# Kernel tuning notes

Measured on AMD Instinct MI355X. Metric: run time of the kernel, lower is better.

## Reference

```python
import jax, jax.numpy as jnp
import numpy as np

NUM_TAGS = 512
START_TAG = 510
STOP_TAG = 511
BATCH = 128
SEQ_LEN = 512
NEG_INF = -10000.0


def setup_inputs() -> dict:
    key = jax.random.key(0)
    k1, k2, k3 = jax.random.split(key, 3)
    inputs = jax.random.normal(k1, (BATCH, SEQ_LEN, NUM_TAGS), dtype=jnp.float32)
    tags = jax.random.randint(k2, (BATCH, SEQ_LEN), 0, NUM_TAGS)
    transitions = jax.random.normal(k3, (NUM_TAGS, NUM_TAGS), dtype=jnp.float32)
    # match the torch __init__ sentinel masking of the transition matrix
    transitions = transitions.at[START_TAG, :].set(NEG_INF)
    transitions = transitions.at[:, STOP_TAG].set(NEG_INF)
    return {"inputs": inputs, "tags": tags, "transitions": transitions}


def reference(inputs, tags, transitions):
    # inputs: [B, S, T] emission scores; transitions[j, i] = score of i -> j
    B, S, T = inputs.shape
    alpha0 = jnp.full((B, T), NEG_INF, dtype=inputs.dtype)
    alpha0 = alpha0.at[:, START_TAG].set(0.0)

    def step(alpha, emit):
        # alpha: [B, T] (prev tags), emit: [B, T] (next tags)
        # scores[b, next, prev] = alpha[b, prev] + transitions[next, prev]
        scores = alpha[:, None, :] + transitions[None, :, :]  # [B, T, T]
        new_alpha = emit + jax.nn.logsumexp(scores, axis=-1)   # [B, T]
        return new_alpha, None

    emits = jnp.moveaxis(inputs, 1, 0)  # [S, B, T]
    alpha, _ = jax.lax.scan(step, alpha0, emits)

    terminal = alpha + transitions[STOP_TAG][None, :]  # [B, T]
    losses = jax.nn.logsumexp(terminal, axis=-1)       # [B]
    return jnp.sum(losses)
```

## Files before the change

kernel.cpp:

```cpp
#include <hip/hip_runtime.h>
#include <stdint.h>

#define NTAGS 512
#define STAG 510
#define PTAG 511
#define SEQ 512
#define L2E 1.4426950408889634f
#define LN2 0.6931471805599453f

typedef int   v8i __attribute__((ext_vector_type(8)));
typedef float v4f __attribute__((ext_vector_type(4)));

__device__ __forceinline__ float fexp2(float x) {
#if __has_builtin(__builtin_amdgcn_exp2f)
    return __builtin_amdgcn_exp2f(x);
#else
    float r; asm("v_exp_f32 %0, %1\n\ts_nop 1" : "=v"(r) : "v"(x)); return r;
#endif
}

#define DPPMAX(X, CTRL) fmaxf((X), __int_as_float(__builtin_amdgcn_update_dpp( \
    0, __float_as_int(X), (CTRL), 0xF, 0xF, false)))

#define STEP_SYNC() asm volatile("s_waitcnt lgkmcnt(0)\n\ts_barrier" ::: "memory")

#define WS_SC   196608
#define WS_PART 204800

__global__ void crf_setup_k(const float* __restrict__ trans, uint8_t* __restrict__ ws)
{
    int t = blockIdx.x * blockDim.x + threadIdx.x;
    int n = t >> 4, KB = t & 15;
    const float* row = trans + n * NTAGS;
    int wq = KB >> 1, h = KB & 1;
    float v[32]; float mx = -3.0e38f;
    #pragma unroll
    for (int k = 0; k < 32; ++k) {
        int p = wq*64 + (k & 3)*16 + h*8 + (k >> 2);
        v[k] = row[p]; mx = fmaxf(mx, v[k]);
    }
    int e = (int)floorf(mx * L2E - 2.90689059f);
    int byt = e + 127; byt = byt < 0 ? 0 : (byt > 254 ? 254 : byt);
    float eeff = (float)(byt - 127);
    uint32_t out[6] = {0u,0u,0u,0u,0u,0u};
    #pragma unroll
    for (int k = 0; k < 32; ++k) {
        float q = exp2f(v[k] * L2E - eeff);
        int code;
        if      (q < 2.0f) code = (int)(q * 8.0f + 0.5f);
        else if (q < 4.0f) code = 16 + (int)((q - 2.0f) * 4.0f + 0.5f);
        else               code = 24 + (int)((q - 4.0f) * 2.0f + 0.5f);
        code = code > 31 ? 31 : code;
        int bp = 6*k, d = bp >> 5, off = bp & 31;
        out[d] |= (uint32_t)code << off;
        if (off > 26) out[d+1] |= (uint32_t)code >> (32 - off);
    }
    uint32_t* E6 = (uint32_t*)ws;
    int base = (n*16 + KB) * 6;
    #pragma unroll
    for (int d = 0; d < 6; ++d) E6[base + d] = out[d];
    ws[WS_SC + n*16 + (KB & 3)*4 + (KB >> 2)] = (uint8_t)byt;
}

__global__ __launch_bounds__(512, 2) void crf_main_k(
    const float* __restrict__ inp, const float* __restrict__ trans,
    const uint8_t* __restrict__ ws, float* __restrict__ part)
{
    __shared__ uint8_t aqb[2*8192];
    __shared__ uint8_t scb[2*256];
    __shared__ int     mxp[2*16];
    __shared__ float   mxb[16*8];
    __shared__ float   ssum[16*8];
    __shared__ float   Gb[16];

    const int tid = threadIdx.x;
    const int w = tid >> 6, l = tid & 63, c = l & 15, g = l >> 4;
    const int wg = blockIdx.x;
    const int b0 = g * 4;

    v8i Bf[16];
    int esc[4];
    #pragma unroll
    for (int i = 0; i < 4; ++i) {
        const int n = (w*4 + i)*16 + c;
        esc[i] = *(const int*)(ws + WS_SC + n*16 + g*4);
        #pragma unroll
        for (int kk = 0; kk < 4; ++kk) {
            const uint2* p2 = (const uint2*)((const uint32_t*)ws + (n*16 + kk*4 + g)*6);
            uint2 d0 = p2[0], d1 = p2[1], d2 = p2[2];
            v8i bv;
            bv[0]=(int)d0.x; bv[1]=(int)d0.y; bv[2]=(int)d1.x;
            bv[3]=(int)d1.y; bv[4]=(int)d2.x; bv[5]=(int)d2.y;
            bv[6]=0; bv[7]=0;
            Bf[i*4 + kk] = bv;
        }
    }
    #pragma unroll
    for (int i = 0; i < 16; ++i) asm volatile("" : "+v"(Bf[i]));
    #pragma unroll
    for (int i = 0; i < 4; ++i)  asm volatile("" : "+v"(esc[i]));

    const float* ep[4];
    #pragma unroll
    for (int j = 0; j < 4; ++j)
        ep[j] = inp + (size_t)(wg*16 + b0 + j) * (SEQ*NTAGS) + w*64 + c;

    int aqoff[4], scoffw[4];
    #pragma unroll
    for (int j = 0; j < 4; ++j) {
        int bb = b0 + j;
        aqoff[j] = bb*128 + (((w*4 + (c>>2)) ^ (bb & 7)) << 2) + (c & 3);
        int B_ = w*2 + (c>>3);
        scoffw[j] = bb*16 + ((B_ & 3)<<2) + (B_>>2);
    }

#define QUANT_STORE(J, V0, V1, V2, V3, RJ, AQ, SC) do { \
    float bm_ = fmaxf(fmaxf(V0, V1), fmaxf(V2, V3)); \
    bm_ = DPPMAX(bm_, 0xB1); bm_ = DPPMAX(bm_, 0x4E); bm_ = DPPMAX(bm_, 0x141); \
    int be_ = (int)((__float_as_uint(bm_) >> 23) & 255u) - 127; \
    be_ = be_ < -60 ? -60 : be_; \
    float qs_ = __int_as_float((uint32_t)(133 - be_) << 23); \
    int t_ = __builtin_amdgcn_cvt_pk_fp8_f32((V0)*qs_, (V1)*qs_, 0, false); \
    t_ = __builtin_amdgcn_cvt_pk_fp8_f32((V2)*qs_, (V3)*qs_, t_, true); \
    ((uint32_t*)(AQ))[aqoff[J]] = (uint32_t)t_; \
    if ((c & 7) == 0) { \
        int sb_ = 121 + be_ - (RJ); sb_ = sb_ < 0 ? 0 : (sb_ > 254 ? 254 : sb_); \
        (SC)[scoffw[J]] = (uint8_t)sb_; \
    } \
    bmout_[J] = bm_; \
} while (0)

    float vv[4][4];
    {
        float tr[4];
        #pragma unroll
        for (int i = 0; i < 4; ++i) tr[i] = trans[(w*64 + i*16 + c)*NTAGS + STAG];
        #pragma unroll
        for (int j = 0; j < 4; ++j) {
            #pragma unroll
            for (int i = 0; i < 4; ++i)
                vv[j][i] = ep[j][i*16] + tr[i];
        }
    }
    float Mj[4];
    #pragma unroll
    for (int j = 0; j < 4; ++j) {
        float m = fmaxf(fmaxf(vv[j][0], vv[j][1]), fmaxf(vv[j][2], vv[j][3]));
        #pragma unroll
        for (int msk = 1; msk <= 8; msk <<= 1) m = fmaxf(m, __shfl_xor(m, msk, 64));
        if (c == 0) mxb[(b0 + j)*8 + w] = m;
    }
    __syncthreads();
    float G[4];
    #pragma unroll
    for (int j = 0; j < 4; ++j) {
        float m = -3.0e38f;
        #pragma unroll
        for (int k = 0; k < 8; ++k) m = fmaxf(m, mxb[(b0 + j)*8 + k]);
        Mj[j] = m;
        G[j] = m * L2E;
    }
    {
        float bmout_[4];
        uint8_t* AQ = aqb + 8192; uint8_t* SC = scb + 256;
        #pragma unroll
        for (int j = 0; j < 4; ++j) {
            float q0 = fexp2((vv[j][0] - Mj[j]) * L2E);
            float q1 = fexp2((vv[j][1] - Mj[j]) * L2E);
            float q2 = fexp2((vv[j][2] - Mj[j]) * L2E);
            float q3 = fexp2((vv[j][3] - Mj[j]) * L2E);
            QUANT_STORE(j, q0, q1, q2, q3, 0, AQ, SC);
        }
        (void)bmout_;
    }
    if (w == 0 && c == 0) { int4 z; z.x=0; z.y=0; z.z=0; z.w=0; *(int4*)&mxp[16 + g*4] = z; }

    float emn[4][4];
    #pragma unroll
    for (int j = 0; j < 4; ++j) ep[j] += NTAGS;
    #pragma unroll
    for (int j = 0; j < 4; ++j) {
        #pragma unroll
        for (int i = 0; i < 4; ++i) emn[j][i] = ep[j][i*16];
    }
    __syncthreads();

    int aoffA[8];
    #pragma unroll
    for (int kk = 0; kk < 4; ++kk) {
        aoffA[2*kk]   = c*32 + ((kk*8 + g*2)     ^ (c & 7));
        aoffA[2*kk+1] = c*32 + ((kk*8 + g*2 + 1) ^ (c & 7));
    }
    const int scoff = c*16 + g*4;

#define MFMA_K(KK) do { \
    v8i A_; \
    *(int4*)&A_       = aq4[aoffA[2*(KK)]]; \
    *(((int4*)&A_)+1) = aq4[aoffA[2*(KK)+1]]; \
    D[0] = __builtin_amdgcn_mfma_scale_f32_16x16x128_f8f6f4(A_, Bf[0*4+(KK)], D[0], 0, 2, (KK), scA, (KK), esc[0]); \
    D[1] = __builtin_amdgcn_mfma_scale_f32_16x16x128_f8f6f4(A_, Bf[1*4+(KK)], D[1], 0, 2, (KK), scA, (KK), esc[1]); \
    D[2] = __builtin_amdgcn_mfma_scale_f32_16x16x128_f8f6f4(A_, Bf[2*4+(KK)], D[2], 0, 2, (KK), scA, (KK), esc[2]); \
    D[3] = __builtin_amdgcn_mfma_scale_f32_16x16x128_f8f6f4(A_, Bf[3*4+(KK)], D[3], 0, 2, (KK), scA, (KK), esc[3]); \
} while (0)

    for (int s = 1; s < SEQ; ++s) {
        const int cur = s & 1, nxt = cur ^ 1;

        float emx[4][4];
        #pragma unroll
        for (int j = 0; j < 4; ++j) {
            #pragma unroll
            for (int i = 0; i < 4; ++i) emx[j][i] = fexp2(emn[j][i] * L2E);
        }
        if (s < SEQ - 1) {
            #pragma unroll
            for (int j = 0; j < 4; ++j) ep[j] += NTAGS;
            #pragma unroll
            for (int j = 0; j < 4; ++j) {
                #pragma unroll
                for (int i = 0; i < 4; ++i) emn[j][i] = ep[j][i*16];
            }
        }

        int4 Pv = *(const int4*)&mxp[cur*16 + g*4];
        uint32_t scA = *(const uint32_t*)(scb + cur*256 + scoff);
        const int4* aq4 = (const int4*)(aqb + cur*8192);

        v4f D[4];
        #pragma unroll
        for (int i = 0; i < 4; ++i) { D[i][0]=0.f; D[i][1]=0.f; D[i][2]=0.f; D[i][3]=0.f; }
        __builtin_amdgcn_s_setprio(1);
        MFMA_K(0); MFMA_K(1); MFMA_K(2); MFMA_K(3);
        __builtin_amdgcn_s_setprio(0);

        if (s < SEQ - 1) {
            int Rj[4];
            #pragma unroll
            for (int j = 0; j < 4; ++j) {
                Rj[j] = ((const int*)&Pv)[j] + 8;
                G[j] += (float)Rj[j];
            }
            float bmout_[4];
            uint8_t* AQ = aqb + nxt*8192; uint8_t* SC = scb + nxt*256;
            #pragma unroll
            for (int j = 0; j < 4; ++j) {
                float v0 = D[0][j] * emx[j][0];
                float v1 = D[1][j] * emx[j][1];
                float v2 = D[2][j] * emx[j][2];
                float v3 = D[3][j] * emx[j][3];
                QUANT_STORE(j, v0, v1, v2, v3, Rj[j], AQ, SC);
            }
            if (w == 0) {
                int4 post;
                #pragma unroll
                for (int j = 0; j < 4; ++j) {
                    float bb = DPPMAX(bmout_[j], 0x140);
                    int be0 = (int)((__float_as_uint(bb) >> 23) & 255u) - 127;
                    ((int*)&post)[j] = be0 - Rj[j];
                }
                if (c == 0) *(int4*)&mxp[nxt*16 + g*4] = post;
            }
            STEP_SYNC();
        } else {
            float ts[4];
            #pragma unroll
            for (int i = 0; i < 4; ++i) ts[i] = trans[PTAG*NTAGS + w*64 + i*16 + c];
            float x[4][4];
            #pragma unroll
            for (int j = 0; j < 4; ++j) {
                #pragma unroll
                for (int i = 0; i < 4; ++i)
                    x[j][i] = __log2f(D[i][j]) + (emn[j][i] + ts[i]) * L2E;
            }
            #pragma unroll
            for (int j = 0; j < 4; ++j) {
                float m = fmaxf(fmaxf(x[j][0], x[j][1]), fmaxf(x[j][2], x[j][3]));
                #pragma unroll
                for (int msk = 1; msk <= 8; msk <<= 1) m = fmaxf(m, __shfl_xor(m, msk, 64));
                if (c == 0) mxb[(b0 + j)*8 + w] = m;
            }
            if (w == 0 && c == 0) {
                #pragma unroll
                for (int j = 0; j < 4; ++j) Gb[b0 + j] = G[j];
            }
            __syncthreads();
            #pragma unroll
            for (int j = 0; j < 4; ++j) {
                float XM = -3.0e38f;
                #pragma unroll
                for (int k = 0; k < 8; ++k) XM = fmaxf(XM, mxb[(b0 + j)*8 + k]);
                float sj = fexp2(x[j][0] - XM) + fexp2(x[j][1] - XM)
                         + fexp2(x[j][2] - XM) + fexp2(x[j][3] - XM);
                #pragma unroll
                for (int msk = 1; msk <= 8; msk <<= 1) sj += __shfl_xor(sj, msk, 64);
                if (c == 0) ssum[(b0 + j)*8 + w] = sj;
            }
            __syncthreads();
            if (tid < 16) {
                float S = 0.f, XM = -3.0e38f;
                #pragma unroll
                for (int k = 0; k < 8; ++k) { S += ssum[tid*8 + k]; XM = fmaxf(XM, mxb[tid*8 + k]); }
                part[wg*16 + tid] = LN2 * (Gb[tid] + XM + __log2f(S));
            }
        }
    }
#undef MFMA_K
#undef QUANT_STORE
}

__global__ void crf_final_k(const float* __restrict__ part, float* __restrict__ out)
{
    int t = threadIdx.x;
    float vsum = part[t] + part[t + 64];
    #pragma unroll
    for (int off = 32; off; off >>= 1) vsum += __shfl_down(vsum, off, 64);
    if (t == 0) out[0] = vsum;
}

extern "C" void kernel_launch(void* const* d_in, const int* in_sizes, int n_in,
                              void* d_out, int out_size, void* d_ws, size_t ws_size,
                              hipStream_t stream)
{
    (void)in_sizes; (void)n_in; (void)out_size; (void)ws_size;
    const float* inp   = (const float*)d_in[0];
    const float* trans = (const float*)d_in[2];
    uint8_t* ws = (uint8_t*)d_ws;
    float* part = (float*)(ws + WS_PART);

    crf_setup_k<<<64, 128, 0, stream>>>(trans, ws);
    crf_main_k<<<8, 512, 0, stream>>>(inp, trans, ws, part);
    crf_final_k<<<1, 64, 0, stream>>>(part, (float*)d_out);
}
```

Baseline: 790.9 us.

## Replace per-block A scales with constant scale and per-row exponent folded into emissions

Removes the per-8-column block-exponent scaling of the alpha vector (the scb shared array, its per-step writes and reads, and the per-lane block max reductions). Each batch row now gets one power-of-two shift, derived from the previous step's row max plus a margin, which is folded into the emission exponent via an fma. The fp8 A operand uses a fixed scale constant and values are clamped at 448. This shortens the per-step critical path (fewer DPP reductions and LDS traffic), but only wave 0 still computes the row max, and the coarser per-row scaling risks precision loss or underflow for small entries.

```diff
diff --git a/kernel.cpp b/kernel.cpp
--- a/kernel.cpp
+++ b/kernel.cpp
@@ -7,6 +7,7 @@
 #define SEQ 512
 #define L2E 1.4426950408889634f
 #define LN2 0.6931471805599453f
+#define MARGIN 13
 
 typedef int   v8i __attribute__((ext_vector_type(8)));
 typedef float v4f __attribute__((ext_vector_type(4)));
@@ -67,7 +68,6 @@
     const uint8_t* __restrict__ ws, float* __restrict__ part)
 {
     __shared__ uint8_t aqb[2*8192];
-    __shared__ uint8_t scb[2*256];
     __shared__ int     mxp[2*16];
     __shared__ float   mxb[16*8];
     __shared__ float   ssum[16*8];
@@ -77,6 +77,7 @@
     const int w = tid >> 6, l = tid & 63, c = l & 15, g = l >> 4;
     const int wg = blockIdx.x;
     const int b0 = g * 4;
+    const int SCA = 0x78787878;
 
     v8i Bf[16];
     int esc[4];
@@ -105,30 +106,12 @@
     for (int j = 0; j < 4; ++j)
         ep[j] = inp + (size_t)(wg*16 + b0 + j) * (SEQ*NTAGS) + w*64 + c;
 
-    int aqoff[4], scoffw[4];
+    int aqoff[4];
     #pragma unroll
     for (int j = 0; j < 4; ++j) {
         int bb = b0 + j;
         aqoff[j] = bb*128 + (((w*4 + (c>>2)) ^ (bb & 7)) << 2) + (c & 3);
-        int B_ = w*2 + (c>>3);
-        scoffw[j] = bb*16 + ((B_ & 3)<<2) + (B_>>2);
-    }
-
-#define QUANT_STORE(J, V0, V1, V2, V3, RJ, AQ, SC) do { \
-    float bm_ = fmaxf(fmaxf(V0, V1), fmaxf(V2, V3)); \
-    bm_ = DPPMAX(bm_, 0xB1); bm_ = DPPMAX(bm_, 0x4E); bm_ = DPPMAX(bm_, 0x141); \
-    int be_ = (int)((__float_as_uint(bm_) >> 23) & 255u) - 127; \
-    be_ = be_ < -60 ? -60 : be_; \
-    float qs_ = __int_as_float((uint32_t)(133 - be_) << 23); \
-    int t_ = __builtin_amdgcn_cvt_pk_fp8_f32((V0)*qs_, (V1)*qs_, 0, false); \
-    t_ = __builtin_amdgcn_cvt_pk_fp8_f32((V2)*qs_, (V3)*qs_, t_, true); \
-    ((uint32_t*)(AQ))[aqoff[J]] = (uint32_t)t_; \
-    if ((c & 7) == 0) { \
-        int sb_ = 121 + be_ - (RJ); sb_ = sb_ < 0 ? 0 : (sb_ > 254 ? 254 : sb_); \
-        (SC)[scoffw[J]] = (uint8_t)sb_; \
-    } \
-    bmout_[J] = bm_; \
-} while (0)
+    }
 
     float vv[4][4];
     {
@@ -161,17 +144,17 @@
         G[j] = m * L2E;
     }
     {
-        float bmout_[4];
-        uint8_t* AQ = aqb + 8192; uint8_t* SC = scb + 256;
+        uint32_t* AQ = (uint32_t*)(aqb + 8192);
         #pragma unroll
         for (int j = 0; j < 4; ++j) {
-            float q0 = fexp2((vv[j][0] - Mj[j]) * L2E);
-            float q1 = fexp2((vv[j][1] - Mj[j]) * L2E);
-            float q2 = fexp2((vv[j][2] - Mj[j]) * L2E);
-            float q3 = fexp2((vv[j][3] - Mj[j]) * L2E);
-            QUANT_STORE(j, q0, q1, q2, q3, 0, AQ, SC);
-        }
-        (void)bmout_;
+            float q0 = fexp2((vv[j][0] - Mj[j]) * L2E + 7.0f);
+            float q1 = fexp2((vv[j][1] - Mj[j]) * L2E + 7.0f);
+            float q2 = fexp2((vv[j][2] - Mj[j]) * L2E + 7.0f);
+            float q3 = fexp2((vv[j][3] - Mj[j]) * L2E + 7.0f);
+            int t_ = __builtin_amdgcn_cvt_pk_fp8_f32(q0, q1, 0, false);
+            t_ = __builtin_amdgcn_cvt_pk_fp8_f32(q2, q3, t_, true);
+            AQ[aqoff[j]] = (uint32_t)t_;
+        }
     }
     if (w == 0 && c == 0) { int4 z; z.x=0; z.y=0; z.z=0; z.w=0; *(int4*)&mxp[16 + g*4] = z; }
 
@@ -191,26 +174,34 @@
         aoffA[2*kk]   = c*32 + ((kk*8 + g*2)     ^ (c & 7));
         aoffA[2*kk+1] = c*32 + ((kk*8 + g*2 + 1) ^ (c & 7));
     }
-    const int scoff = c*16 + g*4;
 
 #define MFMA_K(KK) do { \
     v8i A_; \
     *(int4*)&A_       = aq4[aoffA[2*(KK)]]; \
     *(((int4*)&A_)+1) = aq4[aoffA[2*(KK)+1]]; \
-    D[0] = __builtin_amdgcn_mfma_scale_f32_16x16x128_f8f6f4(A_, Bf[0*4+(KK)], D[0], 0, 2, (KK), scA, (KK), esc[0]); \
-    D[1] = __builtin_amdgcn_mfma_scale_f32_16x16x128_f8f6f4(A_, Bf[1*4+(KK)], D[1], 0, 2, (KK), scA, (KK), esc[1]); \
-    D[2] = __builtin_amdgcn_mfma_scale_f32_16x16x128_f8f6f4(A_, Bf[2*4+(KK)], D[2], 0, 2, (KK), scA, (KK), esc[2]); \
-    D[3] = __builtin_amdgcn_mfma_scale_f32_16x16x128_f8f6f4(A_, Bf[3*4+(KK)], D[3], 0, 2, (KK), scA, (KK), esc[3]); \
+    D[0] = __builtin_amdgcn_mfma_scale_f32_16x16x128_f8f6f4(A_, Bf[0*4+(KK)], D[0], 0, 2, (KK), SCA, (KK), esc[0]); \
+    D[1] = __builtin_amdgcn_mfma_scale_f32_16x16x128_f8f6f4(A_, Bf[1*4+(KK)], D[1], 0, 2, (KK), SCA, (KK), esc[1]); \
+    D[2] = __builtin_amdgcn_mfma_scale_f32_16x16x128_f8f6f4(A_, Bf[2*4+(KK)], D[2], 0, 2, (KK), SCA, (KK), esc[2]); \
+    D[3] = __builtin_amdgcn_mfma_scale_f32_16x16x128_f8f6f4(A_, Bf[3*4+(KK)], D[3], 0, 2, (KK), SCA, (KK), esc[3]); \
 } while (0)
 
     for (int s = 1; s < SEQ; ++s) {
         const int cur = s & 1, nxt = cur ^ 1;
 
+        int4 Pv = *(const int4*)&mxp[cur*16 + g*4];
+        int Rj[4]; float dmj[4];
+        #pragma unroll
+        for (int j = 0; j < 4; ++j) {
+            Rj[j] = ((const int*)&Pv)[j] + MARGIN;
+            dmj[j] = (float)(7 - Rj[j]);
+        }
+
         float emx[4][4];
         #pragma unroll
         for (int j = 0; j < 4; ++j) {
             #pragma unroll
-            for (int i = 0; i < 4; ++i) emx[j][i] = fexp2(emn[j][i] * L2E);
+            for (int i = 0; i < 4; ++i)
+                emx[j][i] = fexp2(fmaf(emn[j][i], L2E, dmj[j]));
         }
         if (s < SEQ - 1) {
             #pragma unroll
@@ -222,8 +213,6 @@
             }
         }
 
-        int4 Pv = *(const int4*)&mxp[cur*16 + g*4];
-        uint32_t scA = *(const uint32_t*)(scb + cur*256 + scoff);
         const int4* aq4 = (const int4*)(aqb + cur*8192);
 
         v4f D[4];
@@ -234,29 +223,33 @@
         __builtin_amdgcn_s_setprio(0);
 
         if (s < SEQ - 1) {
-            int Rj[4];
-            #pragma unroll
-            for (int j = 0; j < 4; ++j) {
-                Rj[j] = ((const int*)&Pv)[j] + 8;
-                G[j] += (float)Rj[j];
-            }
-            float bmout_[4];
-            uint8_t* AQ = aqb + nxt*8192; uint8_t* SC = scb + nxt*256;
-            #pragma unroll
-            for (int j = 0; j < 4; ++j) {
-                float v0 = D[0][j] * emx[j][0];
-                float v1 = D[1][j] * emx[j][1];
-                float v2 = D[2][j] * emx[j][2];
-                float v3 = D[3][j] * emx[j][3];
-                QUANT_STORE(j, v0, v1, v2, v3, Rj[j], AQ, SC);
+            #pragma unroll
+            for (int j = 0; j < 4; ++j) G[j] += (float)Rj[j];
+
+            float vq[4][4];
+            #pragma unroll
+            for (int j = 0; j < 4; ++j) {
+                #pragma unroll
+                for (int i = 0; i < 4; ++i)
+                    vq[j][i] = fminf(D[i][j] * emx[j][i], 448.0f);
+            }
+            uint32_t* AQ = (uint32_t*)(aqb + nxt*8192);
+            #pragma unroll
+            for (int j = 0; j < 4; ++j) {
+                int t_ = __builtin_amdgcn_cvt_pk_fp8_f32(vq[j][0], vq[j][1], 0, false);
+                t_ = __builtin_amdgcn_cvt_pk_fp8_f32(vq[j][2], vq[j][3], t_, true);
+                AQ[aqoff[j]] = (uint32_t)t_;
             }
             if (w == 0) {
                 int4 post;
                 #pragma unroll
                 for (int j = 0; j < 4; ++j) {
-                    float bb = DPPMAX(bmout_[j], 0x140);
-                    int be0 = (int)((__float_as_uint(bb) >> 23) & 255u) - 127;
-                    ((int*)&post)[j] = be0 - Rj[j];
+                    float bm = fmaxf(fmaxf(vq[j][0], vq[j][1]), fmaxf(vq[j][2], vq[j][3]));
+                    bm = DPPMAX(bm, 0xB1); bm = DPPMAX(bm, 0x4E);
+                    bm = DPPMAX(bm, 0x141); bm = DPPMAX(bm, 0x140);
+                    int be = (int)((__float_as_uint(bm) >> 23) & 255u) - 127;
+                    be = be < -30 ? -30 : be;
+                    ((int*)&post)[j] = be - 7;
                 }
                 if (c == 0) *(int4*)&mxp[nxt*16 + g*4] = post;
             }
@@ -305,7 +298,6 @@
         }
     }
 #undef MFMA_K
-#undef QUANT_STORE
 }
 
 __global__ void crf_final_k(const float* __restrict__ part, float* __restrict__ out)
```

Result: faster. 646.4 us (-18.3%).
